# Kernel optimization log

Measured on AMD Instinct MI355X. Metric: run time of the kernel, lower is better.

Reference implementation:

```python
import jax, jax.numpy as jnp
import numpy as np

N = 100000      # num nodes
E = 1600000     # num edges (avg degree 16)
F_IN = 256      # num_node_features
HID = 128       # hid_dim
C = 16          # num_classes


def gcn_conv(x, W, b, src, dst, num_nodes):
    # Linear transform first (PyG GCNConv transforms then aggregates)
    h = x @ W  # [N, out]
    # Symmetric normalization with self-loops already included in src/dst
    ones = jnp.ones_like(dst, dtype=h.dtype)
    deg = jax.ops.segment_sum(ones, dst, num_segments=num_nodes)  # in-degree incl. self-loop
    dinv = jnp.where(deg > 0, jax.lax.rsqrt(deg), 0.0)
    norm = dinv[src] * dinv[dst]                 # [E+N]
    msg = h[src] * norm[:, None]                 # gather + scale
    out = jax.ops.segment_sum(msg, dst, num_segments=num_nodes)  # scatter-add
    return out + b


def setup_inputs() -> dict:
    key = jax.random.key(0)
    k = jax.random.split(key, 4)
    x = jax.random.normal(k[0], (N, F_IN), dtype=jnp.float32)
    edge_index = jax.random.randint(k[1], (2, E), 0, N, dtype=jnp.int32)
    W1 = jax.random.normal(k[2], (F_IN, HID), dtype=jnp.float32) * (1.0 / np.sqrt(F_IN))
    b1 = jnp.zeros((HID,), dtype=jnp.float32)
    W2 = jax.random.normal(k[3], (HID, C), dtype=jnp.float32) * (1.0 / np.sqrt(HID))
    b2 = jnp.zeros((C,), dtype=jnp.float32)
    return {"x": x, "edge_index": edge_index, "W1": W1, "b1": b1, "W2": W2, "b2": b2}


def reference(x, edge_index, W1, b1, W2, b2):
    num_nodes = x.shape[0]
    loop = jnp.arange(num_nodes, dtype=edge_index.dtype)
    src = jnp.concatenate([edge_index[0], loop])  # add self-loops
    dst = jnp.concatenate([edge_index[1], loop])
    h = gcn_conv(x, W1, b1, src, dst, num_nodes)
    h = jax.nn.relu(h)
    # F.dropout(training=self.training): identity in eval mode
    out = gcn_conv(h, W2, b2, src, dst, num_nodes)
    return out
```

## Files before the change

### kernel.cpp

```cpp
#include <hip/hip_runtime.h>
#include <cstddef>

#define CAP 48

typedef short short8 __attribute__((ext_vector_type(8)));
typedef float floatx4 __attribute__((ext_vector_type(4)));

__device__ inline float b2f_lo(unsigned int u) {
  union { unsigned int i; float f; } c;
  c.i = u << 16;
  return c.f;
}
__device__ inline float b2f_hi(unsigned int u) {
  union { unsigned int i; float f; } c;
  c.i = u & 0xFFFF0000u;
  return c.f;
}
__device__ inline unsigned short f2b(float f) {
  union { float f; unsigned int i; } c;
  c.f = f;
  unsigned int u = c.i;
  unsigned int r = (u + 0x7FFFu + ((u >> 16) & 1u)) >> 16;
  return (unsigned short)r;
}
__device__ inline float dinv_of(int c) { return rsqrtf((float)(c + 1)); }

__global__ void k_prep(int* __restrict__ cnt, int N,
                       const float* __restrict__ W1, unsigned short* __restrict__ W1T) {
  int i = blockIdx.x * 256 + threadIdx.x;
  if (i < N) cnt[i] = 0;
  if (i < 256 * 128) {
    int k = i >> 7, n = i & 127;
    W1T[n * 256 + k] = f2b(W1[i]);
  }
}

__global__ __launch_bounds__(256) void k_build_gemm1(
    const int* __restrict__ src, const int* __restrict__ dst, int E, int N,
    int* __restrict__ cnt, int* __restrict__ bucket,
    const float* __restrict__ X, const unsigned short* __restrict__ W1T,
    unsigned short* __restrict__ H1, int M, int gblocks, int total) {
  __shared__ unsigned short As[64 * 40];
  __shared__ unsigned short Bs[128 * 40];

  const unsigned int idx = blockIdx.x;
  const unsigned int gBefore = (idx * (unsigned int)gblocks) / (unsigned int)total;
  const unsigned int gAfter = ((idx + 1) * (unsigned int)gblocks) / (unsigned int)total;
  const bool isGemm = (gAfter > gBefore);

  if (!isGemm) {
    const int bi = (int)(idx - gBefore);
    const int tb = bi * 256 + (int)threadIdx.x;
    const int i0 = tb * 4;
    if (i0 >= E) return;
    if (i0 + 3 < E) {
      int4 d4 = *(const int4*)(dst + i0);
      int4 s4 = *(const int4*)(src + i0);
      int p0 = atomicAdd(&cnt[d4.x], 1);
      int p1 = atomicAdd(&cnt[d4.y], 1);
      int p2 = atomicAdd(&cnt[d4.z], 1);
      int p3 = atomicAdd(&cnt[d4.w], 1);
      if (p0 < CAP) bucket[(size_t)d4.x * CAP + p0] = s4.x;
      if (p1 < CAP) bucket[(size_t)d4.y * CAP + p1] = s4.y;
      if (p2 < CAP) bucket[(size_t)d4.z * CAP + p2] = s4.z;
      if (p3 < CAP) bucket[(size_t)d4.w * CAP + p3] = s4.w;
    } else {
      for (int i = i0; i < E; ++i) {
        int d = dst[i], s = src[i];
        int pos = atomicAdd(&cnt[d], 1);
        if (pos < CAP) bucket[(size_t)d * CAP + pos] = s;
      }
    }
    return;
  }

  const int bid = (int)gBefore;
  const int tid = threadIdx.x;
  const int wave = tid >> 6;
  const int lane = tid & 63;
  const int quad = lane >> 4;
  const int l16 = lane & 15;
  const int row0 = bid * 64;
  const int n0 = wave * 32;

  floatx4 acc[4][2];
#pragma unroll
  for (int r = 0; r < 4; r++)
#pragma unroll
    for (int c = 0; c < 2; c++) acc[r][c] = (floatx4){0.f, 0.f, 0.f, 0.f};

  for (int k0 = 0; k0 < 256; k0 += 32) {
    {
      int r = tid >> 2;
      int q = tid & 3;
      int gr = row0 + r;
      float4 v0 = make_float4(0.f, 0.f, 0.f, 0.f), v1 = v0;
      if (gr < M) {
        const float4* xp = (const float4*)(X + (size_t)gr * 256 + k0 + q * 8);
        v0 = xp[0];
        v1 = xp[1];
      }
      unsigned short tmp[8];
      tmp[0] = f2b(v0.x); tmp[1] = f2b(v0.y); tmp[2] = f2b(v0.z); tmp[3] = f2b(v0.w);
      tmp[4] = f2b(v1.x); tmp[5] = f2b(v1.y); tmp[6] = f2b(v1.z); tmp[7] = f2b(v1.w);
      *(uint4*)(As + r * 40 + q * 8) = *(const uint4*)(tmp);
    }
    {
      int n = tid >> 1;
      int half = (tid & 1) * 16;
      const uint4* wp = (const uint4*)(W1T + (size_t)n * 256 + k0 + half);
      uint4 w0 = wp[0];
      uint4 w1 = wp[1];
      unsigned short* p = Bs + n * 40 + half;
      *(uint4*)(p) = w0;
      *(uint4*)(p + 8) = w1;
    }
    __syncthreads();

    short8 afr[4], bfr[2];
#pragma unroll
    for (int r = 0; r < 4; r++)
      afr[r] = *(const short8*)(As + (r * 16 + l16) * 40 + quad * 8);
#pragma unroll
    for (int c = 0; c < 2; c++)
      bfr[c] = *(const short8*)(Bs + (n0 + c * 16 + l16) * 40 + quad * 8);
#pragma unroll
    for (int r = 0; r < 4; r++)
#pragma unroll
      for (int c = 0; c < 2; c++)
        acc[r][c] = __builtin_amdgcn_mfma_f32_16x16x32_bf16(afr[r], bfr[c], acc[r][c], 0, 0, 0);
    __syncthreads();
  }

#pragma unroll
  for (int r = 0; r < 4; r++) {
#pragma unroll
    for (int c = 0; c < 2; c++) {
      int col = n0 + c * 16 + l16;
#pragma unroll
      for (int i = 0; i < 4; i++) {
        int gr = row0 + r * 16 + quad * 4 + i;
        if (gr < M) H1[(size_t)gr * 128 + col] = f2b(acc[r][c][i]);
      }
    }
  }
}

__global__ __launch_bounds__(256) void k_agg1g2(const unsigned short* __restrict__ H1,
                                                const int* __restrict__ cnt,
                                                const int* __restrict__ bucket,
                                                const float* __restrict__ b1,
                                                const float* __restrict__ W2,
                                                unsigned short* __restrict__ H2, int N) {
  __shared__ float Ws[16 * 130];
  {
    int t = threadIdx.x;
    if (t < 128) {
      const float4* s4 = (const float4*)(W2 + t * 16);
      float4 w0 = s4[0], w1 = s4[1], w2v = s4[2], w3 = s4[3];
      float* d = Ws + (t >> 3) * 130 + (t & 7) * 16;
      d[0] = w0.x;  d[1] = w0.y;  d[2] = w0.z;  d[3] = w0.w;
      d[4] = w1.x;  d[5] = w1.y;  d[6] = w1.z;  d[7] = w1.w;
      d[8] = w2v.x; d[9] = w2v.y; d[10] = w2v.z; d[11] = w2v.w;
      d[12] = w3.x; d[13] = w3.y; d[14] = w3.z; d[15] = w3.w;
    }
  }
  __syncthreads();

  const int lane = threadIdx.x & 15;
  const int node = blockIdx.x * 16 + (threadIdx.x >> 4);
  if (node >= N) return;
  const int cn = cnt[node];
  const float di = dinv_of(cn);
  const float wself = di * di;
  const int deg = min(cn, CAP);
  const int* bk = bucket + (size_t)node * CAP;

  int idx0 = (lane < deg) ? bk[lane] : 0;
  int idx1 = (lane + 16 < deg) ? bk[lane + 16] : 0;
  int idx2 = (lane + 32 < deg) ? bk[lane + 32] : 0;
  float dv0 = (lane < deg) ? dinv_of(cnt[idx0]) : 0.f;
  float dv1 = (lane + 16 < deg) ? dinv_of(cnt[idx1]) : 0.f;
  float dv2 = (lane + 32 < deg) ? dinv_of(cnt[idx2]) : 0.f;

  uint4 hs = ((const uint4*)(H1 + (size_t)node * 128))[lane];
  float a0 = b2f_lo(hs.x) * wself, a1 = b2f_hi(hs.x) * wself;
  float a2 = b2f_lo(hs.y) * wself, a3 = b2f_hi(hs.y) * wself;
  float a4 = b2f_lo(hs.z) * wself, a5 = b2f_hi(hs.z) * wself;
  float a6 = b2f_lo(hs.w) * wself, a7 = b2f_hi(hs.w) * wself;
  float c0 = 0.f, c1 = 0.f, c2 = 0.f, c3 = 0.f, c4 = 0.f, c5 = 0.f, c6 = 0.f, c7 = 0.f;

  for (int j = 0; j < deg; j += 4) {
    int b = j >> 4;
    int idxB = (b == 0) ? idx0 : ((b == 1) ? idx1 : idx2);
    float dvB = (b == 0) ? dv0 : ((b == 1) ? dv1 : dv2);
    int base = j & 15;
    int s0 = __shfl(idxB, base + 0, 16);
    int s1 = __shfl(idxB, base + 1, 16);
    int s2 = __shfl(idxB, base + 2, 16);
    int s3 = __shfl(idxB, base + 3, 16);
    float w0 = __shfl(dvB, base + 0, 16) * di;
    float w1 = __shfl(dvB, base + 1, 16) * di;
    float w2 = __shfl(dvB, base + 2, 16) * di;
    float w3 = __shfl(dvB, base + 3, 16) * di;
    uint4 v0 = ((const uint4*)(H1 + (size_t)s0 * 128))[lane];
    uint4 v1 = ((const uint4*)(H1 + (size_t)s1 * 128))[lane];
    uint4 v2 = ((const uint4*)(H1 + (size_t)s2 * 128))[lane];
    uint4 v3 = ((const uint4*)(H1 + (size_t)s3 * 128))[lane];
    a0 += b2f_lo(v0.x) * w0; a1 += b2f_hi(v0.x) * w0;
    a2 += b2f_lo(v0.y) * w0; a3 += b2f_hi(v0.y) * w0;
    a4 += b2f_lo(v0.z) * w0; a5 += b2f_hi(v0.z) * w0;
    a6 += b2f_lo(v0.w) * w0; a7 += b2f_hi(v0.w) * w0;
    c0 += b2f_lo(v1.x) * w1; c1 += b2f_hi(v1.x) * w1;
    c2 += b2f_lo(v1.y) * w1; c3 += b2f_hi(v1.y) * w1;
    c4 += b2f_lo(v1.z) * w1; c5 += b2f_hi(v1.z) * w1;
    c6 += b2f_lo(v1.w) * w1; c7 += b2f_hi(v1.w) * w1;
    a0 += b2f_lo(v2.x) * w2; a1 += b2f_hi(v2.x) * w2;
    a2 += b2f_lo(v2.y) * w2; a3 += b2f_hi(v2.y) * w2;
    a4 += b2f_lo(v2.z) * w2; a5 += b2f_hi(v2.z) * w2;
    a6 += b2f_lo(v2.w) * w2; a7 += b2f_hi(v2.w) * w2;
    a0 += b2f_lo(v3.x) * w3; a1 += b2f_hi(v3.x) * w3;
    a2 += b2f_lo(v3.y) * w3; a3 += b2f_hi(v3.y) * w3;
    a4 += b2f_lo(v3.z) * w3; a5 += b2f_hi(v3.z) * w3;
    a6 += b2f_lo(v3.w) * w3; a7 += b2f_hi(v3.w) * w3;
  }
  a0 += c0; a1 += c1; a2 += c2; a3 += c3;
  a4 += c4; a5 += c5; a6 += c6; a7 += c7;

  float4 bb0 = ((const float4*)b1)[lane * 2];
  float4 bb1 = ((const float4*)b1)[lane * 2 + 1];
  float av[8];
  av[0] = fmaxf(a0 + bb0.x, 0.f); av[1] = fmaxf(a1 + bb0.y, 0.f);
  av[2] = fmaxf(a2 + bb0.z, 0.f); av[3] = fmaxf(a3 + bb0.w, 0.f);
  av[4] = fmaxf(a4 + bb1.x, 0.f); av[5] = fmaxf(a5 + bb1.y, 0.f);
  av[6] = fmaxf(a6 + bb1.z, 0.f); av[7] = fmaxf(a7 + bb1.w, 0.f);

  float2 p2[8];
#pragma unroll
  for (int c = 0; c < 8; c++) p2[c] = make_float2(0.f, 0.f);
  const float* wl = Ws + lane * 130;
#pragma unroll
  for (int i = 0; i < 8; i++) {
    const float a = av[i];
    const float2* wr = (const float2*)(wl + i * 16);
#pragma unroll
    for (int c = 0; c < 8; c++) {
      float2 wv = wr[c];
      p2[c].x += a * wv.x;
      p2[c].y += a * wv.y;
    }
  }
  float p[16];
#pragma unroll
  for (int c = 0; c < 8; c++) { p[2 * c] = p2[c].x; p[2 * c + 1] = p2[c].y; }

  float k8[8];
  {
    const bool hi = (lane & 8) != 0;
#pragma unroll
    for (int i = 0; i < 8; i++) {
      float keep = hi ? p[8 + i] : p[i];
      float send = hi ? p[i] : p[8 + i];
      k8[i] = keep + __shfl_xor(send, 8, 16);
    }
  }
  float k4[4];
  {
    const bool hi = (lane & 4) != 0;
#pragma unroll
    for (int i = 0; i < 4; i++) {
      float keep = hi ? k8[4 + i] : k8[i];
      float send = hi ? k8[i] : k8[4 + i];
      k4[i] = keep + __shfl_xor(send, 4, 16);
    }
  }
  float k2[2];
  {
    const bool hi = (lane & 2) != 0;
#pragma unroll
    for (int i = 0; i < 2; i++) {
      float keep = hi ? k4[2 + i] : k4[i];
      float send = hi ? k4[i] : k4[2 + i];
      k2[i] = keep + __shfl_xor(send, 2, 16);
    }
  }
  float v;
  {
    const bool hi = (lane & 1) != 0;
    float keep = hi ? k2[1] : k2[0];
    float send = hi ? k2[0] : k2[1];
    v = keep + __shfl_xor(send, 1, 16);
  }
  H2[(size_t)node * 16 + lane] = f2b(v);
}

__global__ __launch_bounds__(256) void k_agg2(const unsigned short* __restrict__ H2,
                                              const int* __restrict__ cnt,
                                              const int* __restrict__ bucket,
                                              const float* __restrict__ b2,
                                              float* __restrict__ out, int N) {
  const int t = threadIdx.x;
  const int half = t & 1;
  const int par = (t >> 1) & 1;
  const int node = blockIdx.x * 64 + (t >> 2);
  if (node >= N) return;
  const int cn = cnt[node];
  const float di = dinv_of(cn);
  const float wself = di * di;
  const int deg = min(cn, CAP);
  const int* bk = bucket + (size_t)node * CAP;

  float a0 = 0.f, a1 = 0.f, a2 = 0.f, a3 = 0.f, a4 = 0.f, a5 = 0.f, a6 = 0.f, a7 = 0.f;
  if (par == 0) {
    uint4 h = ((const uint4*)(H2 + (size_t)node * 16))[half];
    a0 = b2f_lo(h.x) * wself; a1 = b2f_hi(h.x) * wself;
    a2 = b2f_lo(h.y) * wself; a3 = b2f_hi(h.y) * wself;
    a4 = b2f_lo(h.z) * wself; a5 = b2f_hi(h.z) * wself;
    a6 = b2f_lo(h.w) * wself; a7 = b2f_hi(h.w) * wself;
  }

  for (int j = par * 4; j < deg; j += 8) {
    int4 s4 = *(const int4*)(bk + j);
    int s0 = s4.x;
    int s1 = (j + 1 < deg) ? s4.y : 0;
    int s2 = (j + 2 < deg) ? s4.z : 0;
    int s3 = (j + 3 < deg) ? s4.w : 0;
    float w0 = dinv_of(cnt[s0]) * di;
    float w1 = (j + 1 < deg) ? dinv_of(cnt[s1]) * di : 0.f;
    float w2 = (j + 2 < deg) ? dinv_of(cnt[s2]) * di : 0.f;
    float w3 = (j + 3 < deg) ? dinv_of(cnt[s3]) * di : 0.f;
    uint4 v0 = ((const uint4*)(H2 + (size_t)s0 * 16))[half];
    uint4 v1 = ((const uint4*)(H2 + (size_t)s1 * 16))[half];
    uint4 v2 = ((const uint4*)(H2 + (size_t)s2 * 16))[half];
    uint4 v3 = ((const uint4*)(H2 + (size_t)s3 * 16))[half];
    a0 += b2f_lo(v0.x) * w0 + b2f_lo(v1.x) * w1 + b2f_lo(v2.x) * w2 + b2f_lo(v3.x) * w3;
    a1 += b2f_hi(v0.x) * w0 + b2f_hi(v1.x) * w1 + b2f_hi(v2.x) * w2 + b2f_hi(v3.x) * w3;
    a2 += b2f_lo(v0.y) * w0 + b2f_lo(v1.y) * w1 + b2f_lo(v2.y) * w2 + b2f_lo(v3.y) * w3;
    a3 += b2f_hi(v0.y) * w0 + b2f_hi(v1.y) * w1 + b2f_hi(v2.y) * w2 + b2f_hi(v3.y) * w3;
    a4 += b2f_lo(v0.z) * w0 + b2f_lo(v1.z) * w1 + b2f_lo(v2.z) * w2 + b2f_lo(v3.z) * w3;
    a5 += b2f_hi(v0.z) * w0 + b2f_hi(v1.z) * w1 + b2f_hi(v2.z) * w2 + b2f_hi(v3.z) * w3;
    a6 += b2f_lo(v0.w) * w0 + b2f_lo(v1.w) * w1 + b2f_lo(v2.w) * w2 + b2f_lo(v3.w) * w3;
    a7 += b2f_hi(v0.w) * w0 + b2f_hi(v1.w) * w1 + b2f_hi(v2.w) * w2 + b2f_hi(v3.w) * w3;
  }

  a0 += __shfl_xor(a0, 2); a1 += __shfl_xor(a1, 2);
  a2 += __shfl_xor(a2, 2); a3 += __shfl_xor(a3, 2);
  a4 += __shfl_xor(a4, 2); a5 += __shfl_xor(a5, 2);
  a6 += __shfl_xor(a6, 2); a7 += __shfl_xor(a7, 2);

  if (par == 0) {
    float4 bb0 = ((const float4*)b2)[half * 2];
    float4 bb1 = ((const float4*)b2)[half * 2 + 1];
    float4 o0 = make_float4(a0 + bb0.x, a1 + bb0.y, a2 + bb0.z, a3 + bb0.w);
    float4 o1 = make_float4(a4 + bb1.x, a5 + bb1.y, a6 + bb1.z, a7 + bb1.w);
    ((float4*)(out + (size_t)node * 16))[half * 2] = o0;
    ((float4*)(out + (size_t)node * 16))[half * 2 + 1] = o1;
  }
}


extern "C" void kernel_launch(void* const* d_in, const int* in_sizes, int n_in,
                              void* d_out, int out_size, void* d_ws, size_t ws_size,
                              hipStream_t stream) {
  const float* x  = (const float*)d_in[0];
  const int* eidx = (const int*)d_in[1];
  const float* W1 = (const float*)d_in[2];
  const float* b1 = (const float*)d_in[3];
  const float* W2 = (const float*)d_in[4];
  const float* b2 = (const float*)d_in[5];
  float* out = (float*)d_out;

  const int HID = in_sizes[3];
  const int F   = in_sizes[2] / HID;
  const int N   = in_sizes[0] / F;
  const int E   = in_sizes[1] / 2;
  (void)n_in; (void)out_size; (void)ws_size;

  const int* src = eidx;
  const int* dst = eidx + E;

  char* base = (char*)d_ws;
  size_t off = 0;
  auto alloc = [&](size_t bytes) -> char* {
    char* p = base + off;
    off = (off + bytes + 255) & ~(size_t)255;
    return p;
  };
  int*            cnt    = (int*)alloc((size_t)N * 4);
  int*            bucket = (int*)alloc((size_t)N * CAP * 4);
  unsigned short* w1t    = (unsigned short*)alloc((size_t)256 * 128 * 2);
  unsigned short* h1     = (unsigned short*)alloc((size_t)N * 128 * 2);
  unsigned short* h2     = (unsigned short*)alloc((size_t)N * 16 * 2);

  const int nbN = (N + 255) / 256;
  const int gblocks = (N + 63) / 64;
  const int quads = (E + 3) / 4;
  const int nbuild = (quads + 255) / 256;
  const int total = nbuild + gblocks;

  hipLaunchKernelGGL(k_prep, dim3(nbN), dim3(256), 0, stream, cnt, N, W1, w1t);
  hipLaunchKernelGGL(k_build_gemm1, dim3(total), dim3(256), 0, stream,
                     src, dst, E, N, cnt, bucket, x, w1t, h1, N, gblocks, total);
  hipLaunchKernelGGL(k_agg1g2, dim3((N + 15) / 16), dim3(256), 0, stream, h1, cnt, bucket,
                     b1, W2, h2, N);
  hipLaunchKernelGGL(k_agg2, dim3((N + 63) / 64), dim3(256), 0, stream, h2, cnt, bucket,
                     b2, out, N);
}
```

Baseline: 318.5 us.

## Split fused build/GEMM kernel, prefetch GEMM tiles, partition bucket build by destination range

Splits the fused edge-bucket build and first GEMM back into two kernels. The GEMM now register-prefetches the next K-slice of X and W1T while the current slice is computed. The bucket build now uses 8 destination-range groups: each group scans all edges but only does atomics and writes for destinations in its range, so each pass's atomic and scatter traffic hits a smaller, more cache-resident region. The cost is reading the edge list eight times, an extra launch, and losing overlap between the GEMM and the build.

After: 337.7 us. 6.0% more time.

```diff
diff --git a/kernel.cpp b/kernel.cpp
--- a/kernel.cpp
+++ b/kernel.cpp
@@ -35,85 +35,58 @@
   }
 }
 
-__global__ __launch_bounds__(256) void k_build_gemm1(
-    const int* __restrict__ src, const int* __restrict__ dst, int E, int N,
-    int* __restrict__ cnt, int* __restrict__ bucket,
+__global__ __launch_bounds__(256) void k_gemm1(
     const float* __restrict__ X, const unsigned short* __restrict__ W1T,
-    unsigned short* __restrict__ H1, int M, int gblocks, int total) {
+    unsigned short* __restrict__ H1, int M) {
   __shared__ unsigned short As[64 * 40];
   __shared__ unsigned short Bs[128 * 40];
-
-  const unsigned int idx = blockIdx.x;
-  const unsigned int gBefore = (idx * (unsigned int)gblocks) / (unsigned int)total;
-  const unsigned int gAfter = ((idx + 1) * (unsigned int)gblocks) / (unsigned int)total;
-  const bool isGemm = (gAfter > gBefore);
-
-  if (!isGemm) {
-    const int bi = (int)(idx - gBefore);
-    const int tb = bi * 256 + (int)threadIdx.x;
-    const int i0 = tb * 4;
-    if (i0 >= E) return;
-    if (i0 + 3 < E) {
-      int4 d4 = *(const int4*)(dst + i0);
-      int4 s4 = *(const int4*)(src + i0);
-      int p0 = atomicAdd(&cnt[d4.x], 1);
-      int p1 = atomicAdd(&cnt[d4.y], 1);
-      int p2 = atomicAdd(&cnt[d4.z], 1);
-      int p3 = atomicAdd(&cnt[d4.w], 1);
-      if (p0 < CAP) bucket[(size_t)d4.x * CAP + p0] = s4.x;
-      if (p1 < CAP) bucket[(size_t)d4.y * CAP + p1] = s4.y;
-      if (p2 < CAP) bucket[(size_t)d4.z * CAP + p2] = s4.z;
-      if (p3 < CAP) bucket[(size_t)d4.w * CAP + p3] = s4.w;
-    } else {
-      for (int i = i0; i < E; ++i) {
-        int d = dst[i], s = src[i];
-        int pos = atomicAdd(&cnt[d], 1);
-        if (pos < CAP) bucket[(size_t)d * CAP + pos] = s;
-      }
-    }
-    return;
-  }
-
-  const int bid = (int)gBefore;
   const int tid = threadIdx.x;
   const int wave = tid >> 6;
   const int lane = tid & 63;
   const int quad = lane >> 4;
   const int l16 = lane & 15;
-  const int row0 = bid * 64;
+  const int row0 = blockIdx.x * 64;
   const int n0 = wave * 32;
 
+  const int ar = tid >> 2;
+  const int aq = tid & 3;
+  const int agr = row0 + ar;
+  const int agc = (agr < M) ? agr : 0;
+  const float* xrow = X + (size_t)agc * 256 + aq * 8;
+  const int bn = tid >> 1;
+  const int bh = (tid & 1) * 16;
+  const unsigned short* wrow = W1T + (size_t)bn * 256 + bh;
+
   floatx4 acc[4][2];
 #pragma unroll
   for (int r = 0; r < 4; r++)
 #pragma unroll
     for (int c = 0; c < 2; c++) acc[r][c] = (floatx4){0.f, 0.f, 0.f, 0.f};
 
-  for (int k0 = 0; k0 < 256; k0 += 32) {
-    {
-      int r = tid >> 2;
-      int q = tid & 3;
-      int gr = row0 + r;
-      float4 v0 = make_float4(0.f, 0.f, 0.f, 0.f), v1 = v0;
-      if (gr < M) {
-        const float4* xp = (const float4*)(X + (size_t)gr * 256 + k0 + q * 8);
-        v0 = xp[0];
-        v1 = xp[1];
-      }
-      unsigned short tmp[8];
-      tmp[0] = f2b(v0.x); tmp[1] = f2b(v0.y); tmp[2] = f2b(v0.z); tmp[3] = f2b(v0.w);
-      tmp[4] = f2b(v1.x); tmp[5] = f2b(v1.y); tmp[6] = f2b(v1.z); tmp[7] = f2b(v1.w);
-      *(uint4*)(As + r * 40 + q * 8) = *(const uint4*)(tmp);
-    }
-    {
-      int n = tid >> 1;
-      int half = (tid & 1) * 16;
-      const uint4* wp = (const uint4*)(W1T + (size_t)n * 256 + k0 + half);
-      uint4 w0 = wp[0];
-      uint4 w1 = wp[1];
-      unsigned short* p = Bs + n * 40 + half;
-      *(uint4*)(p) = w0;
-      *(uint4*)(p + 8) = w1;
+  float4 cv0 = ((const float4*)xrow)[0];
+  float4 cv1 = ((const float4*)xrow)[1];
+  uint4 cw0 = ((const uint4*)wrow)[0];
+  uint4 cw1 = ((const uint4*)wrow)[1];
+
+#pragma unroll
+  for (int kc = 0; kc < 8; kc++) {
+    unsigned short tmp[8];
+    tmp[0] = f2b(cv0.x); tmp[1] = f2b(cv0.y); tmp[2] = f2b(cv0.z); tmp[3] = f2b(cv0.w);
+    tmp[4] = f2b(cv1.x); tmp[5] = f2b(cv1.y); tmp[6] = f2b(cv1.z); tmp[7] = f2b(cv1.w);
+    *(uint4*)(As + ar * 40 + aq * 8) = *(const uint4*)(tmp);
+    unsigned short* p = Bs + bn * 40 + bh;
+    *(uint4*)(p) = cw0;
+    *(uint4*)(p + 8) = cw1;
+
+    float4 nv0, nv1;
+    uint4 nw0, nw1;
+    if (kc < 7) {
+      const float* xn = xrow + (kc + 1) * 32;
+      nv0 = ((const float4*)xn)[0];
+      nv1 = ((const float4*)xn)[1];
+      const unsigned short* wn = wrow + (kc + 1) * 32;
+      nw0 = ((const uint4*)wn)[0];
+      nw1 = ((const uint4*)wn)[1];
     }
     __syncthreads();
 
@@ -130,6 +103,8 @@
       for (int c = 0; c < 2; c++)
         acc[r][c] = __builtin_amdgcn_mfma_f32_16x16x32_bf16(afr[r], bfr[c], acc[r][c], 0, 0, 0);
     __syncthreads();
+
+    cv0 = nv0; cv1 = nv1; cw0 = nw0; cw1 = nw1;
   }
 
 #pragma unroll
@@ -143,6 +118,40 @@
         if (gr < M) H1[(size_t)gr * 128 + col] = f2b(acc[r][c][i]);
       }
     }
+  }
+}
+
+__global__ __launch_bounds__(256) void k_build(const int* __restrict__ src,
+                                               const int* __restrict__ dst, int E, int N,
+                                               int* __restrict__ cnt,
+                                               int* __restrict__ bucket) {
+  const int g = blockIdx.x & 7;
+  const int w = blockIdx.x >> 3;
+  const int S = (N + 7) >> 3;
+  const int lo = g * S;
+  const int hi = min(N, lo + S);
+  const int T = (gridDim.x >> 3) * 256;
+  const int tb = w * 256 + (int)threadIdx.x;
+  const int E4 = E & ~3;
+
+  for (int i0 = tb * 4; i0 < E4; i0 += T * 4) {
+    int4 d4 = *(const int4*)(dst + i0);
+    int4 s4 = *(const int4*)(src + i0);
+    int p0 = CAP, p1 = CAP, p2 = CAP, p3 = CAP;
+    if (d4.x >= lo && d4.x < hi) p0 = atomicAdd(&cnt[d4.x], 1);
+    if (d4.y >= lo && d4.y < hi) p1 = atomicAdd(&cnt[d4.y], 1);
+    if (d4.z >= lo && d4.z < hi) p2 = atomicAdd(&cnt[d4.z], 1);
+    if (d4.w >= lo && d4.w < hi) p3 = atomicAdd(&cnt[d4.w], 1);
+    if (p0 < CAP) bucket[(size_t)d4.x * CAP + p0] = s4.x;
+    if (p1 < CAP) bucket[(size_t)d4.y * CAP + p1] = s4.y;
+    if (p2 < CAP) bucket[(size_t)d4.z * CAP + p2] = s4.z;
+    if (p3 < CAP) bucket[(size_t)d4.w * CAP + p3] = s4.w;
+  }
+  if (g == 0 && tb < E - E4) {
+    int i = E4 + tb;
+    int d = dst[i], s = src[i];
+    int pos = atomicAdd(&cnt[d], 1);
+    if (pos < CAP) bucket[(size_t)d * CAP + pos] = s;
   }
 }
 
@@ -394,13 +403,10 @@
 
   const int nbN = (N + 255) / 256;
   const int gblocks = (N + 63) / 64;
-  const int quads = (E + 3) / 4;
-  const int nbuild = (quads + 255) / 256;
-  const int total = nbuild + gblocks;
 
   hipLaunchKernelGGL(k_prep, dim3(nbN), dim3(256), 0, stream, cnt, N, W1, w1t);
-  hipLaunchKernelGGL(k_build_gemm1, dim3(total), dim3(256), 0, stream,
-                     src, dst, E, N, cnt, bucket, x, w1t, h1, N, gblocks, total);
+  hipLaunchKernelGGL(k_gemm1, dim3(gblocks), dim3(256), 0, stream, x, w1t, h1, N);
+  hipLaunchKernelGGL(k_build, dim3(2048), dim3(256), 0, stream, src, dst, E, N, cnt, bucket);
   hipLaunchKernelGGL(k_agg1g2, dim3((N + 15) / 16), dim3(256), 0, stream, h1, cnt, bucket,
                      b1, W2, h2, N);
   hipLaunchKernelGGL(k_agg2, dim3((N + 63) / 64), dim3(256), 0, stream, h2, cnt, bucket,
```
